# Kernel optimization log

Measured on AMD Instinct MI355X. Metric: run time of the kernel, lower is better.

The kernel has to match this reference:

```python
import jax, jax.numpy as jnp
import numpy as np

EPS = 1e-06


def setup_inputs() -> dict:
    key = jax.random.key(0)
    k1, k2 = jax.random.split(key)
    N, C, H, W = 256, 3, 256, 256
    preds = jax.random.normal(k1, (N, C, H, W), dtype=jnp.float32)
    targets = jax.random.normal(k2, (N, C, H, W), dtype=jnp.float32)
    return {"preds": preds, "targets": targets}


def reference(preds, targets):
    N = preds.shape[0]
    # Flatten to [N, D] as in torch's .view(len, -1)
    Z = targets.reshape(N, -1)  # targets first, matching the torch call order
    B = preds.reshape(N, -1)
    Z_c = Z - jnp.mean(Z, axis=1, keepdims=True)
    B_c = B - jnp.mean(B, axis=1, keepdims=True)
    # Full N x N cross-correlation matrix (faithful to original), then diagonal
    num = jnp.einsum('nd,md->nm', Z_c, B_c)
    Z_norm = jnp.linalg.norm(Z_c, axis=1, keepdims=True)  # [N,1]
    B_norm = jnp.linalg.norm(B_c, axis=1, keepdims=True)  # [N,1]
    denom = Z_norm @ B_norm.T  # [N,N]
    pearson = num / (denom + EPS)
    corr = jnp.diagonal(pearson)  # [N]
    return jnp.mean(corr)  # reduction='mean'
```

## Files before the change

kernel.cpp:

```cpp
#include <hip/hip_runtime.h>


typedef float f4 __attribute__((ext_vector_type(4)));

constexpr int NROWS  = 256;
constexpr int D      = 3 * 256 * 256;
constexpr int D4     = D / 4;
constexpr int CHUNKS = 32;
constexpr int TPB1   = 256;
constexpr int C4     = D4 / CHUNKS;
constexpr int BATCH  = C4 / TPB1;
constexpr double EPS = 1e-6;

__global__ __launch_bounds__(TPB1) void partial_kernel(
        const f4* __restrict__ preds,
        const f4* __restrict__ targets,
        double* __restrict__ partials)
{
    const int  blk   = blockIdx.x;
    const int  row   = blk / CHUNKS;
    const int  chunk = blk % CHUNKS;
    const int  tid   = threadIdx.x;
    const long base  = (long)row * D4 + (long)chunk * C4 + tid;

    f4 z4[BATCH], b4[BATCH];
    #pragma unroll
    for (int u = 0; u < BATCH; ++u) {
        const long idx = base + (long)u * TPB1;
        b4[u] = __builtin_nontemporal_load(&preds[idx]);
        z4[u] = __builtin_nontemporal_load(&targets[idx]);
    }

    double sZ = 0.0, sB = 0.0, sZZ = 0.0, sBB = 0.0, sZB = 0.0;
    #pragma unroll
    for (int u = 0; u < BATCH; ++u) {
        double z, b;
        z = (double)z4[u].x; b = (double)b4[u].x;
        sZ += z; sB += b; sZZ = fma(z,z,sZZ); sBB = fma(b,b,sBB); sZB = fma(z,b,sZB);
        z = (double)z4[u].y; b = (double)b4[u].y;
        sZ += z; sB += b; sZZ = fma(z,z,sZZ); sBB = fma(b,b,sBB); sZB = fma(z,b,sZB);
        z = (double)z4[u].z; b = (double)b4[u].z;
        sZ += z; sB += b; sZZ = fma(z,z,sZZ); sBB = fma(b,b,sBB); sZB = fma(z,b,sZB);
        z = (double)z4[u].w; b = (double)b4[u].w;
        sZ += z; sB += b; sZZ = fma(z,z,sZZ); sBB = fma(b,b,sBB); sZB = fma(z,b,sZB);
    }

    #pragma unroll
    for (int off = 32; off > 0; off >>= 1) {
        sZ  += __shfl_down(sZ,  off);
        sB  += __shfl_down(sB,  off);
        sZZ += __shfl_down(sZZ, off);
        sBB += __shfl_down(sBB, off);
        sZB += __shfl_down(sZB, off);
    }

    constexpr int NWAVES = TPB1 / 64;
    __shared__ double sm[5][NWAVES];
    const int wave = tid >> 6;
    const int lane = tid & 63;
    if (lane == 0) {
        sm[0][wave] = sZ;  sm[1][wave] = sB;
        sm[2][wave] = sZZ; sm[3][wave] = sBB;
        sm[4][wave] = sZB;
    }
    __syncthreads();

    if (tid == 0) {
        double* out = partials + (long)blk * 5;
        #pragma unroll
        for (int k = 0; k < 5; ++k) {
            double acc = 0.0;
            #pragma unroll
            for (int w = 0; w < NWAVES; ++w) acc += sm[k][w];
            out[k] = acc;
        }
    }
}

__global__ __launch_bounds__(NROWS) void finish_kernel(
        const double* __restrict__ partials, float* __restrict__ out)
{
    const int r = threadIdx.x;
    double tZ = 0, tB = 0, tZZ = 0, tBB = 0, tZB = 0;
    const double* p = partials + (long)r * CHUNKS * 5;
    #pragma unroll
    for (int c = 0; c < CHUNKS; ++c) {
        tZ  += p[c * 5 + 0];
        tB  += p[c * 5 + 1];
        tZZ += p[c * 5 + 2];
        tBB += p[c * 5 + 3];
        tZB += p[c * 5 + 4];
    }
    const double invD = 1.0 / (double)D;
    const double num  = tZB - tZ * tB * invD;
    const double varZ = fmax(tZZ - tZ * tZ * invD, 0.0);
    const double varB = fmax(tBB - tB * tB * invD, 0.0);
    const double den  = sqrt(varZ) * sqrt(varB) + EPS;
    double v = num / den;

    #pragma unroll
    for (int off = 32; off > 0; off >>= 1) v += __shfl_down(v, off);

    __shared__ double sm[NROWS / 64];
    const int wave = r >> 6;
    const int lane = r & 63;
    if (lane == 0) sm[wave] = v;
    __syncthreads();
    if (r == 0) {
        double t = 0.0;
        #pragma unroll
        for (int w = 0; w < NROWS / 64; ++w) t += sm[w];
        out[0] = (float)(t / (double)NROWS);
    }
}

extern "C" void kernel_launch(void* const* d_in, const int* in_sizes, int n_in,
                              void* d_out, int out_size, void* d_ws, size_t ws_size,
                              hipStream_t stream) {
    const f4* preds   = (const f4*)d_in[0];
    const f4* targets = (const f4*)d_in[1];
    double* partials = (double*)d_ws;
    float*  out      = (float*)d_out;

    hipLaunchKernelGGL(partial_kernel, dim3(NROWS * CHUNKS), dim3(TPB1), 0, stream,
                       preds, targets, partials);
    hipLaunchKernelGGL(finish_kernel, dim3(1), dim3(NROWS), 0, stream,
                       partials, out);
}
```

Before: 371.5 us.

## Stage input loads through LDS via async global_load_lds and split final reduction

Input vectors are loaded straight into shared memory with the async global-to-LDS builtin, then read back for the FP64 accumulation. The per-block batch shrinks and the chunk count grows. The single-block finish kernel is replaced by a per-row parallel reduce kernel plus a small mean kernel. This aims to cut register pressure and the serial finish latency, at the cost of an extra launch and an LDS round trip.

```diff
diff --git a/kernel.cpp b/kernel.cpp
--- a/kernel.cpp
+++ b/kernel.cpp
@@ -1,4 +1,5 @@
 #include <hip/hip_runtime.h>
+#include <stdint.h>
 
 
 typedef float f4 __attribute__((ext_vector_type(4)));
@@ -6,42 +7,54 @@
 constexpr int NROWS  = 256;
 constexpr int D      = 3 * 256 * 256;
 constexpr int D4     = D / 4;
-constexpr int CHUNKS = 32;
 constexpr int TPB1   = 256;
-constexpr int C4     = D4 / CHUNKS;
-constexpr int BATCH  = C4 / TPB1;
+constexpr int BATCH  = 4;
+constexpr int C4     = TPB1 * BATCH;
+constexpr int CHUNKS = D4 / C4;
 constexpr double EPS = 1e-6;
+
+__device__ __forceinline__ void async_ld16(const void* g, void* l) {
+    __builtin_amdgcn_global_load_lds(
+        (const __attribute__((address_space(1))) uint32_t*)g,
+        (__attribute__((address_space(3))) uint32_t*)l,
+        16, 0, 2);
+}
 
 __global__ __launch_bounds__(TPB1) void partial_kernel(
         const f4* __restrict__ preds,
         const f4* __restrict__ targets,
         double* __restrict__ partials)
 {
+    __shared__ f4 sBuf[2][BATCH][TPB1];
+
     const int  blk   = blockIdx.x;
     const int  row   = blk / CHUNKS;
     const int  chunk = blk % CHUNKS;
     const int  tid   = threadIdx.x;
-    const long base  = (long)row * D4 + (long)chunk * C4 + tid;
+    const int  w     = tid >> 6;
+    const long G     = (long)row * D4 + (long)chunk * C4;
 
-    f4 z4[BATCH], b4[BATCH];
     #pragma unroll
     for (int u = 0; u < BATCH; ++u) {
-        const long idx = base + (long)u * TPB1;
-        b4[u] = __builtin_nontemporal_load(&preds[idx]);
-        z4[u] = __builtin_nontemporal_load(&targets[idx]);
+        const long gi = G + (long)u * TPB1 + tid;
+        async_ld16(&preds[gi],   &sBuf[0][u][w * 64]);
+        async_ld16(&targets[gi], &sBuf[1][u][w * 64]);
     }
+    __syncthreads();
 
     double sZ = 0.0, sB = 0.0, sZZ = 0.0, sBB = 0.0, sZB = 0.0;
     #pragma unroll
     for (int u = 0; u < BATCH; ++u) {
+        const f4 b4 = sBuf[0][u][tid];
+        const f4 z4 = sBuf[1][u][tid];
         double z, b;
-        z = (double)z4[u].x; b = (double)b4[u].x;
+        z = (double)z4.x; b = (double)b4.x;
         sZ += z; sB += b; sZZ = fma(z,z,sZZ); sBB = fma(b,b,sBB); sZB = fma(z,b,sZB);
-        z = (double)z4[u].y; b = (double)b4[u].y;
+        z = (double)z4.y; b = (double)b4.y;
         sZ += z; sB += b; sZZ = fma(z,z,sZZ); sBB = fma(b,b,sBB); sZB = fma(z,b,sZB);
-        z = (double)z4[u].z; b = (double)b4[u].z;
+        z = (double)z4.z; b = (double)b4.z;
         sZ += z; sB += b; sZZ = fma(z,z,sZZ); sBB = fma(b,b,sBB); sZB = fma(z,b,sZB);
-        z = (double)z4[u].w; b = (double)b4[u].w;
+        z = (double)z4.w; b = (double)b4.w;
         sZ += z; sB += b; sZZ = fma(z,z,sZZ); sBB = fma(b,b,sBB); sZB = fma(z,b,sZB);
     }
 
@@ -56,57 +69,64 @@
 
     constexpr int NWAVES = TPB1 / 64;
     __shared__ double sm[5][NWAVES];
-    const int wave = tid >> 6;
     const int lane = tid & 63;
     if (lane == 0) {
-        sm[0][wave] = sZ;  sm[1][wave] = sB;
-        sm[2][wave] = sZZ; sm[3][wave] = sBB;
-        sm[4][wave] = sZB;
+        sm[0][w] = sZ;  sm[1][w] = sB;
+        sm[2][w] = sZZ; sm[3][w] = sBB;
+        sm[4][w] = sZB;
     }
     __syncthreads();
 
     if (tid == 0) {
         double* out = partials + (long)blk * 5;
         #pragma unroll
-        for (int k = 0; k < 5; ++k) {
-            double acc = 0.0;
-            #pragma unroll
-            for (int w = 0; w < NWAVES; ++w) acc += sm[k][w];
-            out[k] = acc;
-        }
+        for (int k = 0; k < 5; ++k)
+            out[k] = sm[k][0] + sm[k][1] + sm[k][2] + sm[k][3];
     }
 }
 
-__global__ __launch_bounds__(NROWS) void finish_kernel(
-        const double* __restrict__ partials, float* __restrict__ out)
+__global__ __launch_bounds__(64) void row_reduce_kernel(
+        const double* __restrict__ partials, double* __restrict__ rowcorr)
 {
-    const int r = threadIdx.x;
+    const int row = blockIdx.x;
+    const int c   = threadIdx.x;
     double tZ = 0, tB = 0, tZZ = 0, tBB = 0, tZB = 0;
-    const double* p = partials + (long)r * CHUNKS * 5;
+    if (c < CHUNKS) {
+        const double* p = partials + ((long)row * CHUNKS + c) * 5;
+        tZ = p[0]; tB = p[1]; tZZ = p[2]; tBB = p[3]; tZB = p[4];
+    }
     #pragma unroll
-    for (int c = 0; c < CHUNKS; ++c) {
-        tZ  += p[c * 5 + 0];
-        tB  += p[c * 5 + 1];
-        tZZ += p[c * 5 + 2];
-        tBB += p[c * 5 + 3];
-        tZB += p[c * 5 + 4];
+    for (int off = 32; off > 0; off >>= 1) {
+        tZ  += __shfl_down(tZ,  off);
+        tB  += __shfl_down(tB,  off);
+        tZZ += __shfl_down(tZZ, off);
+        tBB += __shfl_down(tBB, off);
+        tZB += __shfl_down(tZB, off);
     }
-    const double invD = 1.0 / (double)D;
-    const double num  = tZB - tZ * tB * invD;
-    const double varZ = fmax(tZZ - tZ * tZ * invD, 0.0);
-    const double varB = fmax(tBB - tB * tB * invD, 0.0);
-    const double den  = sqrt(varZ) * sqrt(varB) + EPS;
-    double v = num / den;
+    if (c == 0) {
+        const double invD = 1.0 / (double)D;
+        const double num  = tZB - tZ * tB * invD;
+        const double varZ = fmax(tZZ - tZ * tZ * invD, 0.0);
+        const double varB = fmax(tBB - tB * tB * invD, 0.0);
+        const double den  = sqrt(varZ) * sqrt(varB) + EPS;
+        rowcorr[row] = num / den;
+    }
+}
 
+__global__ __launch_bounds__(NROWS) void mean_kernel(
+        const double* __restrict__ rowcorr, float* __restrict__ out)
+{
+    const int tid = threadIdx.x;
+    double v = rowcorr[tid];
     #pragma unroll
     for (int off = 32; off > 0; off >>= 1) v += __shfl_down(v, off);
 
     __shared__ double sm[NROWS / 64];
-    const int wave = r >> 6;
-    const int lane = r & 63;
+    const int wave = tid >> 6;
+    const int lane = tid & 63;
     if (lane == 0) sm[wave] = v;
     __syncthreads();
-    if (r == 0) {
+    if (tid == 0) {
         double t = 0.0;
         #pragma unroll
         for (int w = 0; w < NROWS / 64; ++w) t += sm[w];
@@ -120,10 +140,13 @@
     const f4* preds   = (const f4*)d_in[0];
     const f4* targets = (const f4*)d_in[1];
     double* partials = (double*)d_ws;
+    double* rowcorr  = partials + (long)NROWS * CHUNKS * 5;
     float*  out      = (float*)d_out;
 
     hipLaunchKernelGGL(partial_kernel, dim3(NROWS * CHUNKS), dim3(TPB1), 0, stream,
                        preds, targets, partials);
-    hipLaunchKernelGGL(finish_kernel, dim3(1), dim3(NROWS), 0, stream,
-                       partials, out);
+    hipLaunchKernelGGL(row_reduce_kernel, dim3(NROWS), dim3(64), 0, stream,
+                       partials, rowcorr);
+    hipLaunchKernelGGL(mean_kernel, dim3(1), dim3(NROWS), 0, stream,
+                       rowcorr, out);
 }
```

Measured after the change: 358.9 us. 3.4% less time.
